# Optimization experiments

Hardware: AMD Instinct MI355X
Metric: run time of the kernel (lower is better)

The kernel has to match this reference:

```python
import jax, jax.numpy as jnp
import numpy as np

N = 50000      # num nodes
E = 800000     # edges per hypergraph (avg degree 16)
G = 3          # hyper_edge_num
D_IN = 128
D_OUT = 128


def setup_inputs() -> dict:
    key = jax.random.key(0)
    ks = jax.random.split(key, 6)
    company_emb = jax.random.normal(ks[0], (N, D_IN), dtype=jnp.float32)
    # nn.Linear weight [out, in], glorot-ish scaling
    W = jax.random.normal(ks[1], (D_OUT, D_IN), dtype=jnp.float32) / np.sqrt(D_IN).astype(np.float32)
    alpha = jax.random.normal(ks[2], (G, 1), dtype=jnp.float32)
    edge_rows = jax.random.randint(ks[3], (G, E), 0, N, dtype=jnp.int32)
    edge_cols = jax.random.randint(ks[4], (G, E), 0, N, dtype=jnp.int32)
    edge_vals = jax.random.normal(ks[5], (G, E), dtype=jnp.float32)
    return {
        "company_emb": company_emb,
        "W": W,
        "alpha": alpha,
        "edge_rows": edge_rows,
        "edge_cols": edge_cols,
        "edge_vals": edge_vals,
    }


def reference(company_emb, W, alpha, edge_rows, edge_cols, edge_vals):
    # shared dense projection: h = X @ W^T, [N, D_OUT]
    h = company_emb @ W.T

    def spmm(rows, cols, vals):
        # sparse Laplacian (COO) @ h : gather source rows, scale, scatter-add to dest rows
        msg = vals[:, None] * h[cols]                     # [E, D_OUT]
        return jax.ops.segment_sum(msg, rows, num_segments=N)

    aggs = jax.vmap(spmm)(edge_rows, edge_cols, edge_vals)  # [G, N, D_OUT]
    gate = jax.nn.sigmoid(alpha[:, 0])                       # [G]
    # res = sum_g sigmoid(alpha_g) * (L_g @ h)
    return jnp.einsum('g,gnd->nd', gate, aggs)
```

## Files before the change

### kernel.cpp

```cpp
#include <hip/hip_runtime.h>
#include <math.h>

#define NNODES 50000
#define NEDGE  800000
#define NG     3
#define GE     (NG*NEDGE)
#define NBUK   1536
#define OS     (NBUK + 1)
#define CH     4800
#define NBLK   (GE / CH)
#define GBLK   391
#define FGRID  (GBLK + NBLK)
#define STGCAP 1920
#define SCAP   2176

typedef __attribute__((ext_vector_type(8))) short bf16x8;
typedef __attribute__((ext_vector_type(4))) float f32x4;

__device__ __forceinline__ unsigned short f2bf(float f) {
    unsigned u = __float_as_uint(f);
    return (unsigned short)((u + 0x7fffu + ((u >> 16) & 1u)) >> 16);
}

__device__ __forceinline__ int bucket_of(unsigned r) {
    return (int)((r * 96u) / 3125u);
}

__global__ __launch_bounds__(512) void k_front(const float* __restrict__ X,
                                               const float* __restrict__ W,
                                               const int* __restrict__ rows,
                                               const int* __restrict__ cols,
                                               const float* __restrict__ vals,
                                               const float* __restrict__ alpha,
                                               unsigned short* __restrict__ hb16,
                                               uint2* __restrict__ out1,
                                               unsigned short* __restrict__ off1) {
    __shared__ __align__(16) char smem[54144];
    const int t = threadIdx.x;

    if (blockIdx.x < GBLK) {
        uint4* Wl = (uint4*)smem;
        for (int i = t; i < 2048; i += 512) {
            const int nt   = i >> 8;
            const int kc   = (i >> 6) & 3;
            const int lane = i & 63;
            const int n  = nt * 16 + (lane & 15);
            const int k0 = kc * 32 + (lane >> 4) * 8;
            const float* src = W + (size_t)n * 128 + k0;
            float4 a = *(const float4*)(src);
            float4 b = *(const float4*)(src + 4);
            unsigned u0 = (unsigned)f2bf(a.x) | ((unsigned)f2bf(a.y) << 16);
            unsigned u1 = (unsigned)f2bf(a.z) | ((unsigned)f2bf(a.w) << 16);
            unsigned u2 = (unsigned)f2bf(b.x) | ((unsigned)f2bf(b.y) << 16);
            unsigned u3 = (unsigned)f2bf(b.z) | ((unsigned)f2bf(b.w) << 16);
            Wl[i] = make_uint4(u0, u1, u2, u3);
        }
        __syncthreads();

        const int w    = t >> 6;
        const int lane = t & 63;
        const int q    = lane >> 4;
        const int ml   = lane & 15;
        const int m0   = blockIdx.x * 128 + w * 16;

        int xr = m0 + ml; if (xr >= NNODES) xr = NNODES - 1;
        const float* xrow = X + (size_t)xr * 128;

        bf16x8 xf[4];
#pragma unroll
        for (int kc = 0; kc < 4; ++kc) {
            const int k0 = kc * 32 + q * 8;
            float4 a = *(const float4*)(xrow + k0);
            float4 b = *(const float4*)(xrow + k0 + 4);
            bf16x8 v;
            v[0] = (short)f2bf(a.x); v[1] = (short)f2bf(a.y);
            v[2] = (short)f2bf(a.z); v[3] = (short)f2bf(a.w);
            v[4] = (short)f2bf(b.x); v[5] = (short)f2bf(b.y);
            v[6] = (short)f2bf(b.z); v[7] = (short)f2bf(b.w);
            xf[kc] = v;
        }

#pragma unroll
        for (int nt = 0; nt < 8; ++nt) {
            f32x4 acc = {0.f, 0.f, 0.f, 0.f};
#pragma unroll
            for (int kc = 0; kc < 4; ++kc) {
                const bf16x8 wf = *(const bf16x8*)&Wl[(nt * 4 + kc) * 64 + lane];
                acc = __builtin_amdgcn_mfma_f32_16x16x32_bf16(xf[kc], wf, acc, 0, 0, 0);
            }
#pragma unroll
            for (int r = 0; r < 4; ++r) {
                const int row = m0 + q * 4 + r;
                if (row < NNODES)
                    hb16[(size_t)row * 128 + nt * 16 + ml] = f2bf(acc[r]);
            }
        }
    } else {
        uint2*          stg = (uint2*)smem;
        unsigned short* rnk = (unsigned short*)(smem + 38400);
        int*            sA  = (int*)(smem + 48000);
        const int bb    = blockIdx.x - GBLK;
        const int start = bb * CH;

        const float g0 = 1.0f / (1.0f + __expf(-alpha[0]));
        const float g1 = 1.0f / (1.0f + __expf(-alpha[1]));
        const float g2 = 1.0f / (1.0f + __expf(-alpha[2]));

#pragma unroll
        for (int j = 0; j < 3; ++j) sA[t + j * 512] = 0;
        __syncthreads();

        for (int k = t; k < CH; k += 512) {
            const int idx = start + k;
            const int r = rows[idx];
            const int c = cols[idx];
            const float v = vals[idx];
            const float gv = v * (idx < NEDGE ? g0 : (idx < 2 * NEDGE ? g1 : g2));
            uint2 rec;
            rec.x = ((unsigned)r << 16) | (unsigned)c;
            rec.y = __float_as_uint(gv);
            stg[k] = rec;
            rnk[k] = (unsigned short)atomicAdd(&sA[bucket_of((unsigned)r)], 1);
        }
        __syncthreads();

        for (int off = 1; off < 1536; off <<= 1) {
            int v[3];
#pragma unroll
            for (int j = 0; j < 3; ++j) {
                const int i = t + j * 512;
                v[j] = sA[i] + ((i >= off) ? sA[i - off] : 0);
            }
            __syncthreads();
#pragma unroll
            for (int j = 0; j < 3; ++j) sA[t + j * 512] = v[j];
            __syncthreads();
        }

        for (int b = t; b < NBUK; b += 512)
            off1[(size_t)bb * OS + b] = (unsigned short)(b ? sA[b - 1] : 0);
        if (t == 0) off1[(size_t)bb * OS + NBUK] = (unsigned short)sA[NBUK - 1];

        for (int k = t; k < CH; k += 512) {
            const uint2 rec = stg[k];
            const int b = bucket_of(rec.x >> 16);
            const int pos = (b ? sA[b - 1] : 0) + (int)rnk[k];
            out1[(size_t)bb * CH + pos] = rec;
        }
    }
}

__global__ __launch_bounds__(512) void k_agg(const unsigned* __restrict__ hbits,
                                             const uint2* __restrict__ out1,
                                             const unsigned short* __restrict__ off1,
                                             float* __restrict__ out) {
    __shared__ __align__(16) uint2          stg[STGCAP];
    __shared__ __align__(16) unsigned short colS[SCAP];
    __shared__ __align__(16) float          valS[SCAP];
    __shared__ int rh[40], rbase[40], rcur[40];
    __shared__ int sA[512];
    const int t = threadIdx.x;
    const int b = blockIdx.x;

    const int sstart = (b * 3125 + 95) / 96;
    const int send   = ((b + 1) * 3125 + 95) / 96;
    const int width  = send - sstart;

    if (t < 40) rh[t] = 0;

    int s0 = 0, e0 = 0;
    if (t < NBLK) {
        s0 = off1[(size_t)t * OS + b];
        e0 = off1[(size_t)t * OS + b + 1];
    }
    const int len = e0 - s0;
    sA[t] = len;
    __syncthreads();

    for (int off = 1; off < 512; off <<= 1) {
        const int v = sA[t] + ((t >= off) ? sA[t - off] : 0);
        __syncthreads();
        sA[t] = v;
        __syncthreads();
    }
    const int base = sA[t] - len;

    {
        const uint2* seg = out1 + (size_t)t * CH;
        int p = base;
        for (int i = s0; i < e0; ++i, ++p) {
            const uint2 rec = seg[i];
            if (p < STGCAP) {
                stg[p] = rec;
                atomicAdd(&rh[(int)(rec.x >> 16) - sstart], 1);
            }
        }
    }
    __syncthreads();

    if (t < 64) sA[t] = (t < width) ? ((rh[t] + 7) & ~7) : 0;
    __syncthreads();
    for (int off = 1; off < 64; off <<= 1) {
        int v = 0;
        if (t < 64) v = sA[t] + ((t >= off) ? sA[t - off] : 0);
        __syncthreads();
        if (t < 64) sA[t] = v;
        __syncthreads();
    }
    if (t < width) {
        const int rb = sA[t] - ((rh[t] + 7) & ~7);
        rbase[t] = rb;
        rcur[t]  = rb;
    }
    __syncthreads();

    {
        const int lim = (base + len < STGCAP) ? (base + len) : STGCAP;
        for (int k = base; k < lim; ++k) {
            const uint2 rec = stg[k];
            const int lr  = (int)(rec.x >> 16) - sstart;
            const int pos = atomicAdd(&rcur[lr], 1);
            colS[pos] = (unsigned short)(rec.x & 0xffffu);
            valS[pos] = __uint_as_float(rec.y);
        }
    }
    __syncthreads();

    const int w    = t >> 6;
    const int lane = t & 63;
    for (int lr = w; lr < width; lr += 8) {
        const int s   = rbase[lr];
        const int cnt = rh[lr];
        float2 acc = make_float2(0.f, 0.f);
        int i = 0;
        for (; i + 8 <= cnt; i += 8) {
            const uint4  cv = *(const uint4*)&colS[s + i];
            const float4 va = *(const float4*)&valS[s + i];
            const float4 vb = *(const float4*)&valS[s + i + 4];
            unsigned hb[8];
            hb[0] = hbits[(size_t)(cv.x & 0xffffu) * 64 + lane];
            hb[1] = hbits[(size_t)(cv.x >> 16)     * 64 + lane];
            hb[2] = hbits[(size_t)(cv.y & 0xffffu) * 64 + lane];
            hb[3] = hbits[(size_t)(cv.y >> 16)     * 64 + lane];
            hb[4] = hbits[(size_t)(cv.z & 0xffffu) * 64 + lane];
            hb[5] = hbits[(size_t)(cv.z >> 16)     * 64 + lane];
            hb[6] = hbits[(size_t)(cv.w & 0xffffu) * 64 + lane];
            hb[7] = hbits[(size_t)(cv.w >> 16)     * 64 + lane];
            const float vv[8] = {va.x, va.y, va.z, va.w, vb.x, vb.y, vb.z, vb.w};
#pragma unroll
            for (int j = 0; j < 8; ++j) {
                acc.x += vv[j] * __uint_as_float(hb[j] << 16);
                acc.y += vv[j] * __uint_as_float(hb[j] & 0xffff0000u);
            }
        }
        for (; i < cnt; ++i) {
            const unsigned c   = colS[s + i];
            const float    v   = valS[s + i];
            const unsigned hbv = hbits[(size_t)c * 64 + lane];
            acc.x += v * __uint_as_float(hbv << 16);
            acc.y += v * __uint_as_float(hbv & 0xffff0000u);
        }
        const int row = sstart + lr;
        ((float2*)out)[(size_t)row * 64 + lane] = acc;
    }
}

extern "C" void kernel_launch(void* const* d_in, const int* in_sizes, int n_in,
                              void* d_out, int out_size, void* d_ws, size_t ws_size,
                              hipStream_t stream) {
    const float* X     = (const float*)d_in[0];
    const float* W     = (const float*)d_in[1];
    const float* alpha = (const float*)d_in[2];
    const int*   rows  = (const int*)d_in[3];
    const int*   cols  = (const int*)d_in[4];
    const float* vals  = (const float*)d_in[5];
    float* out = (float*)d_out;

    char* ws = (char*)d_ws;
    unsigned*       hbits = (unsigned*)(ws + 0);
    unsigned short* hb16  = (unsigned short*)(ws + 0);
    uint2*          out1  = (uint2*)(ws + 12800000);
    unsigned short* off1  = (unsigned short*)(ws + 32000000);

    hipLaunchKernelGGL(k_front, dim3(FGRID), dim3(512), 0, stream,
                       X, W, rows, cols, vals, alpha, hb16, out1, off1);
    hipLaunchKernelGGL(k_agg, dim3(NBUK), dim3(512), 0, stream,
                       hbits, out1, off1, out);
}
```

Baseline: 220.9 us.

## Stage GEMM output in LDS for coalesced stores, rebalance partition chunks, pad gather rows

The projection kernel now keeps all eight MFMA accumulators, writes bf16 results to per-wave LDS tiles, and stores full 16-byte rows to global memory instead of scattered 2-byte writes. The edge partition moves to 512 chunks of 4688 edges with a clamped tail, so every aggregation thread owns one segment. Row lists in the aggregation are zero-padded to multiples of 8, which removes the scalar tail loop, and the main gather loop is unrolled to 16 in-flight loads. This adds register pressure from 8 accumulators and 16 gather registers, plus extra padded zero-weight gathers.

```diff
diff --git a/kernel.cpp b/kernel.cpp
--- a/kernel.cpp
+++ b/kernel.cpp
@@ -7,8 +7,8 @@
 #define GE     (NG*NEDGE)
 #define NBUK   1536
 #define OS     (NBUK + 1)
-#define CH     4800
-#define NBLK   (GE / CH)
+#define CH     4688
+#define NBLK   512
 #define GBLK   391
 #define FGRID  (GBLK + NBLK)
 #define STGCAP 1920
@@ -35,7 +35,7 @@
                                                unsigned short* __restrict__ hb16,
                                                uint2* __restrict__ out1,
                                                unsigned short* __restrict__ off1) {
-    __shared__ __align__(16) char smem[54144];
+    __shared__ __align__(16) char smem[53024];
     const int t = threadIdx.x;
 
     if (blockIdx.x < GBLK) {
@@ -80,27 +80,44 @@
             xf[kc] = v;
         }
 
-#pragma unroll
-        for (int nt = 0; nt < 8; ++nt) {
-            f32x4 acc = {0.f, 0.f, 0.f, 0.f};
+        f32x4 acc[8];
+#pragma unroll
+        for (int nt = 0; nt < 8; ++nt) acc[nt] = (f32x4){0.f, 0.f, 0.f, 0.f};
+#pragma unroll
+        for (int nt = 0; nt < 8; ++nt)
 #pragma unroll
             for (int kc = 0; kc < 4; ++kc) {
                 const bf16x8 wf = *(const bf16x8*)&Wl[(nt * 4 + kc) * 64 + lane];
-                acc = __builtin_amdgcn_mfma_f32_16x16x32_bf16(xf[kc], wf, acc, 0, 0, 0);
-            }
-#pragma unroll
-            for (int r = 0; r < 4; ++r) {
-                const int row = m0 + q * 4 + r;
-                if (row < NNODES)
-                    hb16[(size_t)row * 128 + nt * 16 + ml] = f2bf(acc[r]);
-            }
+                acc[nt] = __builtin_amdgcn_mfma_f32_16x16x32_bf16(xf[kc], wf, acc[nt], 0, 0, 0);
+            }
+        __syncthreads();
+
+        unsigned short* hst = (unsigned short*)smem + w * 2176;
+#pragma unroll
+        for (int nt = 0; nt < 8; ++nt)
+#pragma unroll
+            for (int r = 0; r < 4; ++r)
+                hst[(q * 4 + r) * 136 + nt * 16 + ml] = f2bf(acc[nt][r]);
+        __syncthreads();
+
+#pragma unroll
+        for (int i = 0; i < 4; ++i) {
+            const int chunk = i * 64 + lane;
+            const int lr    = chunk >> 4;
+            const int cc    = chunk & 15;
+            const int row   = m0 + lr;
+            const uint4 v = *(const uint4*)(hst + lr * 136 + cc * 8);
+            if (row < NNODES)
+                ((uint4*)(hb16 + (size_t)row * 128))[cc] = v;
         }
     } else {
         uint2*          stg = (uint2*)smem;
-        unsigned short* rnk = (unsigned short*)(smem + 38400);
-        int*            sA  = (int*)(smem + 48000);
+        unsigned short* rnk = (unsigned short*)(smem + 37504);
+        int*            sA  = (int*)(smem + 46880);
         const int bb    = blockIdx.x - GBLK;
         const int start = bb * CH;
+        const int end   = (start + CH < GE) ? (start + CH) : GE;
+        const int len   = end - start;
 
         const float g0 = 1.0f / (1.0f + __expf(-alpha[0]));
         const float g1 = 1.0f / (1.0f + __expf(-alpha[1]));
@@ -110,7 +127,7 @@
         for (int j = 0; j < 3; ++j) sA[t + j * 512] = 0;
         __syncthreads();
 
-        for (int k = t; k < CH; k += 512) {
+        for (int k = t; k < len; k += 512) {
             const int idx = start + k;
             const int r = rows[idx];
             const int c = cols[idx];
@@ -137,11 +154,12 @@
             __syncthreads();
         }
 
-        for (int b = t; b < NBUK; b += 512)
-            off1[(size_t)bb * OS + b] = (unsigned short)(b ? sA[b - 1] : 0);
+        if (t < NBUK) off1[(size_t)bb * OS + t] = (unsigned short)(t ? sA[t - 1] : 0);
+        for (int b = t + 512; b < NBUK; b += 512)
+            off1[(size_t)bb * OS + b] = (unsigned short)sA[b - 1];
         if (t == 0) off1[(size_t)bb * OS + NBUK] = (unsigned short)sA[NBUK - 1];
 
-        for (int k = t; k < CH; k += 512) {
+        for (int k = t; k < len; k += 512) {
             const uint2 rec = stg[k];
             const int b = bucket_of(rec.x >> 16);
             const int pos = (b ? sA[b - 1] : 0) + (int)rnk[k];
@@ -150,10 +168,10 @@
     }
 }
 
-__global__ __launch_bounds__(512) void k_agg(const unsigned* __restrict__ hbits,
-                                             const uint2* __restrict__ out1,
-                                             const unsigned short* __restrict__ off1,
-                                             float* __restrict__ out) {
+__global__ __launch_bounds__(512, 8) void k_agg(const unsigned* __restrict__ hbits,
+                                                const uint2* __restrict__ out1,
+                                                const unsigned short* __restrict__ off1,
+                                                float* __restrict__ out) {
     __shared__ __align__(16) uint2          stg[STGCAP];
     __shared__ __align__(16) unsigned short colS[SCAP];
     __shared__ __align__(16) float          valS[SCAP];
@@ -168,11 +186,8 @@
 
     if (t < 40) rh[t] = 0;
 
-    int s0 = 0, e0 = 0;
-    if (t < NBLK) {
-        s0 = off1[(size_t)t * OS + b];
-        e0 = off1[(size_t)t * OS + b + 1];
-    }
+    const int s0 = off1[(size_t)t * OS + b];
+    const int e0 = off1[(size_t)t * OS + b + 1];
     const int len = e0 - s0;
     sA[t] = len;
     __syncthreads();
@@ -208,9 +223,12 @@
         __syncthreads();
     }
     if (t < width) {
-        const int rb = sA[t] - ((rh[t] + 7) & ~7);
+        const int c  = rh[t];
+        const int c8 = (c + 7) & ~7;
+        const int rb = sA[t] - c8;
         rbase[t] = rb;
         rcur[t]  = rb;
+        for (int k = rb + c; k < rb + c8; ++k) { colS[k] = 0; valS[k] = 0.f; }
     }
     __syncthreads();
 
@@ -229,36 +247,61 @@
     const int w    = t >> 6;
     const int lane = t & 63;
     for (int lr = w; lr < width; lr += 8) {
-        const int s   = rbase[lr];
-        const int cnt = rh[lr];
+        const int s    = rbase[lr];
+        const int cnt8 = (rh[lr] + 7) & ~7;
         float2 acc = make_float2(0.f, 0.f);
         int i = 0;
-        for (; i + 8 <= cnt; i += 8) {
-            const uint4  cv = *(const uint4*)&colS[s + i];
-            const float4 va = *(const float4*)&valS[s + i];
-            const float4 vb = *(const float4*)&valS[s + i + 4];
+        for (; i + 16 <= cnt8; i += 16) {
+            const uint4  c0 = *(const uint4*)&colS[s + i];
+            const uint4  c1 = *(const uint4*)&colS[s + i + 8];
+            const float4 v0 = *(const float4*)&valS[s + i];
+            const float4 v1 = *(const float4*)&valS[s + i + 4];
+            const float4 v2 = *(const float4*)&valS[s + i + 8];
+            const float4 v3 = *(const float4*)&valS[s + i + 12];
+            unsigned hb[16];
+            hb[0]  = hbits[(size_t)(c0.x & 0xffffu) * 64 + lane];
+            hb[1]  = hbits[(size_t)(c0.x >> 16)     * 64 + lane];
+            hb[2]  = hbits[(size_t)(c0.y & 0xffffu) * 64 + lane];
+            hb[3]  = hbits[(size_t)(c0.y >> 16)     * 64 + lane];
+            hb[4]  = hbits[(size_t)(c0.z & 0xffffu) * 64 + lane];
+            hb[5]  = hbits[(size_t)(c0.z >> 16)     * 64 + lane];
+            hb[6]  = hbits[(size_t)(c0.w & 0xffffu) * 64 + lane];
+            hb[7]  = hbits[(size_t)(c0.w >> 16)     * 64 + lane];
+            hb[8]  = hbits[(size_t)(c1.x & 0xffffu) * 64 + lane];
+            hb[9]  = hbits[(size_t)(c1.x >> 16)     * 64 + lane];
+            hb[10] = hbits[(size_t)(c1.y & 0xffffu) * 64 + lane];
+            hb[11] = hbits[(size_t)(c1.y >> 16)     * 64 + lane];
+            hb[12] = hbits[(size_t)(c1.z & 0xffffu) * 64 + lane];
+            hb[13] = hbits[(size_t)(c1.z >> 16)     * 64 + lane];
+            hb[14] = hbits[(size_t)(c1.w & 0xffffu) * 64 + lane];
+            hb[15] = hbits[(size_t)(c1.w >> 16)     * 64 + lane];
+            const float vv[16] = {v0.x, v0.y, v0.z, v0.w, v1.x, v1.y, v1.z, v1.w,
+                                  v2.x, v2.y, v2.z, v2.w, v3.x, v3.y, v3.z, v3.w};
+#pragma unroll
+            for (int j = 0; j < 16; ++j) {
+                acc.x += vv[j] * __uint_as_float(hb[j] << 16);
+                acc.y += vv[j] * __uint_as_float(hb[j] & 0xffff0000u);
+            }
+        }
+        if (i < cnt8) {
+            const uint4  c0 = *(const uint4*)&colS[s + i];
+            const float4 v0 = *(const float4*)&valS[s + i];
+            const float4 v1 = *(const float4*)&valS[s + i + 4];
             unsigned hb[8];
-            hb[0] = hbits[(size_t)(cv.x & 0xffffu) * 64 + lane];
-            hb[1] = hbits[(size_t)(cv.x >> 16)     * 64 + lane];
-            hb[2] = hbits[(size_t)(cv.y & 0xffffu) * 64 + lane];
-            hb[3] = hbits[(size_t)(cv.y >> 16)     * 64 + lane];
-            hb[4] = hbits[(size_t)(cv.z & 0xffffu) * 64 + lane];
-            hb[5] = hbits[(size_t)(cv.z >> 16)     * 64 + lane];
-            hb[6] = hbits[(size_t)(cv.w & 0xffffu) * 64 + lane];
-            hb[7] = hbits[(size_t)(cv.w >> 16)     * 64 + lane];
-            const float vv[8] = {va.x, va.y, va.z, va.w, vb.x, vb.y, vb.z, vb.w};
+            hb[0] = hbits[(size_t)(c0.x & 0xffffu) * 64 + lane];
+            hb[1] = hbits[(size_t)(c0.x >> 16)     * 64 + lane];
+            hb[2] = hbits[(size_t)(c0.y & 0xffffu) * 64 + lane];
+            hb[3] = hbits[(size_t)(c0.y >> 16)     * 64 + lane];
+            hb[4] = hbits[(size_t)(c0.z & 0xffffu) * 64 + lane];
+            hb[5] = hbits[(size_t)(c0.z >> 16)     * 64 + lane];
+            hb[6] = hbits[(size_t)(c0.w & 0xffffu) * 64 + lane];
+            hb[7] = hbits[(size_t)(c0.w >> 16)     * 64 + lane];
+            const float vv[8] = {v0.x, v0.y, v0.z, v0.w, v1.x, v1.y, v1.z, v1.w};
 #pragma unroll
             for (int j = 0; j < 8; ++j) {
                 acc.x += vv[j] * __uint_as_float(hb[j] << 16);
                 acc.y += vv[j] * __uint_as_float(hb[j] & 0xffff0000u);
             }
-        }
-        for (; i < cnt; ++i) {
-            const unsigned c   = colS[s + i];
-            const float    v   = valS[s + i];
-            const unsigned hbv = hbits[(size_t)c * 64 + lane];
-            acc.x += v * __uint_as_float(hbv << 16);
-            acc.y += v * __uint_as_float(hbv & 0xffff0000u);
         }
         const int row = sstart + lr;
         ((float2*)out)[(size_t)row * 64 + lane] = acc;
@@ -280,7 +323,7 @@
     unsigned*       hbits = (unsigned*)(ws + 0);
     unsigned short* hb16  = (unsigned short*)(ws + 0);
     uint2*          out1  = (uint2*)(ws + 12800000);
-    unsigned short* off1  = (unsigned short*)(ws + 32000000);
+    unsigned short* off1  = (unsigned short*)(ws + 32002048);
 
     hipLaunchKernelGGL(k_front, dim3(FGRID), dim3(512), 0, stream,
                        X, W, rows, cols, vals, alpha, hb16, out1, off1);
```

After: 219.3 us. No clear change (-0.7%).
